# Kernel optimization log

Measured on AMD Instinct MI355X. Metric: run time of the kernel, lower is better.

The kernel has to match this reference:

```python
import jax, jax.numpy as jnp
import numpy as np

D_MODEL = 1024
N_HEADS = 16
D_K = D_MODEL // N_HEADS
B, S = 4, 2048


def setup_inputs() -> dict:
    key = jax.random.key(0)
    ks = jax.random.split(key, 9)
    sc = 1.0 / np.sqrt(D_MODEL)
    inp = {
        "x": jax.random.normal(ks[0], (B, S, D_MODEL), dtype=jnp.float32),
        # causal mask, broadcastable over batch and heads; 0 -> masked
        "mask": jnp.tril(jnp.ones((S, S), dtype=jnp.int32))[None, None, :, :],
        "Wq": jax.random.normal(ks[1], (D_MODEL, D_MODEL), dtype=jnp.float32) * sc,
        "bq": jax.random.normal(ks[2], (D_MODEL,), dtype=jnp.float32) * sc,
        "Wk": jax.random.normal(ks[3], (D_MODEL, D_MODEL), dtype=jnp.float32) * sc,
        "bk": jax.random.normal(ks[4], (D_MODEL,), dtype=jnp.float32) * sc,
        "Wv": jax.random.normal(ks[5], (D_MODEL, D_MODEL), dtype=jnp.float32) * sc,
        "bv": jax.random.normal(ks[6], (D_MODEL,), dtype=jnp.float32) * sc,
        "Wo": jax.random.normal(ks[7], (D_MODEL, D_MODEL), dtype=jnp.float32) * sc,
        "bo": jax.random.normal(ks[8], (D_MODEL,), dtype=jnp.float32) * sc,
    }
    return inp


def _split_heads(t):
    b, s, _ = t.shape
    return t.reshape(b, s, N_HEADS, D_K).transpose(0, 2, 1, 3)  # [B,H,S,dk]


def reference(x, mask, Wq, bq, Wk, bk, Wv, bv, Wo, bo):
    Q = _split_heads(x @ Wq.T + bq)
    K = _split_heads(x @ Wk.T + bk)
    V = _split_heads(x @ Wv.T + bv)
    scores = jnp.einsum("bhqd,bhkd->bhqk", Q, K) / jnp.sqrt(jnp.float32(D_K))
    scores = jnp.where(mask == 0, jnp.float32(-1e9), scores)
    weights = jax.nn.softmax(scores, axis=-1)
    attn = jnp.einsum("bhqk,bhkd->bhqd", weights, V)  # [B,H,S,dk]
    attn = attn.transpose(0, 2, 1, 3).reshape(x.shape[0], x.shape[1], D_MODEL)
    return attn @ Wo.T + bo
```

## Files before the change

### kernel.cpp

```cpp
#include <hip/hip_runtime.h>
#include <hip/hip_bf16.h>
#include <cstdint>

#define DM   1024
#define NH   16
#define DK   64
#define BB   4
#define SS   2048
#define MTOT (BB * SS)
#define PAD  68

typedef short short8 __attribute__((ext_vector_type(8)));
typedef float f32x4  __attribute__((ext_vector_type(4)));
using u16 = unsigned short;

__device__ inline u16 f2b(float f) {
    union { float f; unsigned int u; } v; v.f = f;
    unsigned int u = v.u;
    u += 0x7fffu + ((u >> 16) & 1u);
    return (u16)(u >> 16);
}
__device__ inline u16 f2b_trunc(float f) {
    union { float f; unsigned int u; } v; v.f = f;
    return (u16)(v.u >> 16);
}
__device__ inline float b2f(u16 s) {
    union { unsigned int u; float f; } v; v.u = ((unsigned int)s) << 16;
    return v.f;
}

__device__ inline void load_lds16(const u16* g, u16* l) {
    __builtin_amdgcn_global_load_lds(
        (const __attribute__((address_space(1))) unsigned int*)g,
        (__attribute__((address_space(3))) unsigned int*)l, 16, 0, 0);
}

struct CvtPtrs {
    const void *x, *Wq, *Wk, *Wv, *Wo, *bq, *bk, *bv, *bo;
    u16 *xb, *Wqb, *Wkb, *Wvb, *Wob, *bqb, *bkb, *bvb, *bob;
};

__global__ void convert_all(CvtPtrs p, int* __restrict__ flag)
{
    __shared__ int cnt;
    if (threadIdx.x == 0) cnt = 0;
    __syncthreads();
    int c = 0;
    for (int i = threadIdx.x; i < 512; i += 256) {
        const int e = (((const u16*)p.x)[i] >> 7) & 0xFF;
        if (e >= 100 && e <= 140) c++;
    }
    atomicAdd(&cnt, c);
    __syncthreads();
    const int isbf = (cnt >= 420) ? 1 : 0;
    if (blockIdx.x == 0 && threadIdx.x == 0) *flag = isbf;
    if (isbf) return;

    const size_t E  = (size_t)MTOT * DM;
    const size_t W1 = (size_t)DM * DM;
    const size_t i = ((size_t)blockIdx.x * blockDim.x + threadIdx.x) * 8;
    const float* s; u16* d; size_t off;
    if (i < E) {
        s = (const float*)p.x; d = p.xb; off = i;
    } else {
        size_t j = i - E;
        if (j < (W1 << 2)) {
            const int w = (int)(j >> 20); off = j & (W1 - 1);
            const float* ss[4] = {(const float*)p.Wq, (const float*)p.Wk,
                                  (const float*)p.Wv, (const float*)p.Wo};
            u16* dd[4] = {p.Wqb, p.Wkb, p.Wvb, p.Wob};
            s = ss[w]; d = dd[w];
        } else {
            j -= (W1 << 2);
            if (j >= 4 * DM) return;
            const int w = (int)(j >> 10); off = j & (DM - 1);
            const float* ss[4] = {(const float*)p.bq, (const float*)p.bk,
                                  (const float*)p.bv, (const float*)p.bo};
            u16* dd[4] = {p.bqb, p.bkb, p.bvb, p.bob};
            s = ss[w]; d = dd[w];
        }
    }
    const float4 f0 = *(const float4*)(s + off);
    const float4 f1 = *(const float4*)(s + off + 4);
    u16 tmp[8] = {f2b(f0.x), f2b(f0.y), f2b(f0.z), f2b(f0.w),
                  f2b(f1.x), f2b(f1.y), f2b(f1.z), f2b(f1.w)};
    *(int4*)(d + off) = *(const int4*)tmp;
}

__device__ __forceinline__
void gemm_body(const u16* __restrict__ A, const u16* __restrict__ Bw,
               const u16* __restrict__ bias, void* __restrict__ out,
               int mode, float scale, int isbf, int m0, int n0,
               u16 (*As)[64], u16 (*Bs)[64])
{
    const int tid  = threadIdx.x;
    const int wave = tid >> 6;
    const int lane = tid & 63;
    const int wm = (wave >> 1) * 64;
    const int wn = (wave & 1) * 64;

    const int lm   = lane & 15;
    const int quad = lane >> 4;
    const int kq   = quad * 8;
    const int rq   = quad * 4;

    const int lrow   = lane >> 3;
    const int lchunk = (lane & 7) ^ lrow;
    const u16* gA = A  + (size_t)(m0 + 8*wave + lrow) * DM + lchunk * 8;
    const u16* gB = Bw + (size_t)(n0 + 8*wave + lrow) * DM + lchunk * 8;
    u16* ldsA = (u16*)((char*)&As[0][0] + wave * 1024);
    u16* ldsB = (u16*)((char*)&Bs[0][0] + wave * 1024);

    f32x4 acc[4][4] = {};

    for (int k0 = 0; k0 < DM; k0 += 64) {
        __syncthreads();
#pragma unroll
        for (int c = 0; c < 4; c++) {
            load_lds16(gA + (size_t)c*32*DM + k0, (u16*)((char*)ldsA + c*4096));
            load_lds16(gB + (size_t)c*32*DM + k0, (u16*)((char*)ldsB + c*4096));
        }
        __syncthreads();

#pragma unroll
        for (int ks = 0; ks < 2; ks++) {
            const int ca = ((ks*4 + quad) ^ (lm & 7)) * 8;
            short8 af[4], bf[4];
#pragma unroll
            for (int i = 0; i < 4; i++) af[i] = *(const short8*)(&As[wm + 16*i + lm][ca]);
#pragma unroll
            for (int j = 0; j < 4; j++) bf[j] = *(const short8*)(&Bs[wn + 16*j + lm][ca]);
#pragma unroll
            for (int i = 0; i < 4; i++)
#pragma unroll
                for (int j = 0; j < 4; j++)
                    acc[i][j] = __builtin_amdgcn_mfma_f32_16x16x32_bf16(af[i], bf[j], acc[i][j], 0, 0, 0);
        }
    }

#pragma unroll
    for (int j = 0; j < 4; j++) {
        const int col = n0 + wn + 16*j + lm;
        const float bv = b2f(bias[col]);
        const int h = col >> 6, d = col & 63;
#pragma unroll
        for (int i = 0; i < 4; i++) {
            if (mode == 2) {
                const int row0 = m0 + wm + 16*i + rq;
                const int b = row0 >> 11, s = row0 & 2047;
                u16 tmp[4];
#pragma unroll
                for (int r = 0; r < 4; r++)
                    tmp[r] = f2b((acc[i][j][r] + bv) * scale);
                const size_t idx = (((size_t)(b*NH + h) * DK) + d) * SS + s;
                *(uint2*)(&((u16*)out)[idx]) = *(const uint2*)tmp;
            } else {
#pragma unroll
                for (int r = 0; r < 4; r++) {
                    const int row = m0 + wm + 16*i + rq + r;
                    const float v = (acc[i][j][r] + bv) * scale;
                    if (mode == 0) {
                        const size_t idx = (size_t)row * DM + col;
                        if (isbf) ((u16*)out)[idx] = f2b(v);
                        else      ((float*)out)[idx] = v;
                    } else {
                        const int b = row >> 11, s = row & 2047;
                        const size_t idx = (((size_t)(b*NH + h) * SS) + s) * DK + d;
                        ((u16*)out)[idx] = f2b(v);
                    }
                }
            }
        }
    }
}

__global__ __launch_bounds__(256)
void gemm_qkv(CvtPtrs p, u16* __restrict__ Qb, u16* __restrict__ Kb,
              u16* __restrict__ Vb, float qscale, const int* __restrict__ flag)
{
    __shared__ __align__(16) u16 As[128][64];
    __shared__ __align__(16) u16 Bs[128][64];
    const int id  = blockIdx.x;
    const int xcd = id & 7;
    const int j   = id >> 3;
    const int m0  = (xcd * 8 + (j & 7)) * 128;
    const int n0  = ((j >> 3) & 7) * 128;
    const int z   = j >> 6;
    const int isbf = *flag;
    const u16* A = isbf ? (const u16*)p.x : p.xb;
    const u16* Bw, *bias; u16* out;
    if (z == 0)      { Bw = isbf ? (const u16*)p.Wq : p.Wqb; bias = isbf ? (const u16*)p.bq : p.bqb; out = Qb; }
    else if (z == 1) { Bw = isbf ? (const u16*)p.Wk : p.Wkb; bias = isbf ? (const u16*)p.bk : p.bkb; out = Kb; }
    else             { Bw = isbf ? (const u16*)p.Wv : p.Wvb; bias = isbf ? (const u16*)p.bv : p.bvb; out = Vb; }
    const int mode  = (z == 2) ? 2 : 1;
    const float sc  = (z == 0) ? qscale : 1.0f;
    gemm_body(A, Bw, bias, out, mode, sc, 1, m0, n0, As, Bs);
}

__global__ __launch_bounds__(256)
void gemm_out(const u16* __restrict__ Ab, CvtPtrs p, void* __restrict__ out,
              const int* __restrict__ flag)
{
    __shared__ __align__(16) u16 As[128][64];
    __shared__ __align__(16) u16 Bs[128][64];
    const int id  = blockIdx.x;
    const int xcd = id & 7;
    const int j   = id >> 3;
    const int m0  = (xcd * 8 + (j & 7)) * 128;
    const int n0  = (j >> 3) * 128;
    const int isbf = *flag;
    const u16* Bw   = isbf ? (const u16*)p.Wo : p.Wob;
    const u16* bias = isbf ? (const u16*)p.bo : p.bob;
    gemm_body(Ab, Bw, bias, out, 0, 1.0f, isbf, m0, n0, As, Bs);
}

__global__ __launch_bounds__(256)
void attn_causal(const u16* __restrict__ Q, const u16* __restrict__ K,
                 const u16* __restrict__ VT, u16* __restrict__ O)
{
    __shared__ __align__(16) u16 Ks[2][64][PAD];
    __shared__ __align__(16) u16 Vs[2][64][PAD];
    __shared__ __align__(16) u16 Ps[128][PAD];

    const int tid  = threadIdx.x;
    const int wave = tid >> 6;
    const int lane = tid & 63;
    const int qx = blockIdx.x;
    const int h = blockIdx.y, b = blockIdx.z;
    const int bh = b * NH + h;

    const u16* Kg = K  + (size_t)bh * SS * DK;
    const u16* Vg = VT + (size_t)bh * DK * SS;

    const int srow = tid >> 3;
    const int scol = (tid & 7) * 8;
    const int lm = lane & 15, quad = lane >> 4, kq = quad * 8, rq = quad * 4;

#pragma unroll
    for (int seg = 0; seg < 2; seg++) {
        const int qt = seg ? (15 - qx) : qx;
        const int q0 = qt * 128;
        const int nt = 2 * (qt + 1);
        const u16* Qg = Q + ((size_t)bh * SS + q0) * DK;

        short8 qa[2][2];
#pragma unroll
        for (int mi = 0; mi < 2; mi++)
#pragma unroll
            for (int ks = 0; ks < 2; ks++)
                qa[mi][ks] = *(const short8*)(&Qg[(size_t)(32*wave + 16*mi + lm) * DK + ks*32 + kq]);

        int4 kv0 = *(const int4*)(&Kg[(size_t)srow * DK + scol]);
        int4 kv1 = *(const int4*)(&Kg[(size_t)(srow + 32) * DK + scol]);
        int4 vv0 = *(const int4*)(&Vg[(size_t)srow * SS + scol]);
        int4 vv1 = *(const int4*)(&Vg[(size_t)(srow + 32) * SS + scol]);
        *(int4*)(&Ks[0][srow][scol])      = kv0;
        *(int4*)(&Ks[0][srow + 32][scol]) = kv1;
        *(int4*)(&Vs[0][srow][scol])      = vv0;
        *(int4*)(&Vs[0][srow + 32][scol]) = vv1;
        __syncthreads();

        kv0 = *(const int4*)(&Kg[(size_t)(64 + srow) * DK + scol]);
        kv1 = *(const int4*)(&Kg[(size_t)(64 + srow + 32) * DK + scol]);
        vv0 = *(const int4*)(&Vg[(size_t)srow * SS + 64 + scol]);
        vv1 = *(const int4*)(&Vg[(size_t)(srow + 32) * SS + 64 + scol]);

        f32x4 o[2][4] = {};
        float lacc[2][4] = {};

        for (int t = 0; t < nt; t++) {
            const int buf = t & 1;
            const int k0 = 64 * t;

            f32x4 sc[2][4] = {};
#pragma unroll
            for (int ks = 0; ks < 2; ks++)
#pragma unroll
                for (int j = 0; j < 4; j++) {
                    const short8 bfr = *(const short8*)(&Ks[buf][16*j + lm][ks*32 + kq]);
                    sc[0][j] = __builtin_amdgcn_mfma_f32_16x16x32_bf16(qa[0][ks], bfr, sc[0][j], 0, 0, 0);
                    sc[1][j] = __builtin_amdgcn_mfma_f32_16x16x32_bf16(qa[1][ks], bfr, sc[1][j], 0, 0, 0);
                }

            if (k0 + 63 > q0 + 32*wave) {
#pragma unroll
                for (int mi = 0; mi < 2; mi++)
#pragma unroll
                    for (int j = 0; j < 4; j++)
#pragma unroll
                        for (int r = 0; r < 4; r++)
                            if (k0 + 16*j + lm > q0 + 32*wave + 16*mi + rq + r)
                                sc[mi][j][r] = -1e30f;
            }

#pragma unroll
            for (int mi = 0; mi < 2; mi++)
#pragma unroll
                for (int j = 0; j < 4; j++)
#pragma unroll
                    for (int r = 0; r < 4; r++) {
                        const float pv = __builtin_amdgcn_exp2f(sc[mi][j][r]);
                        lacc[mi][r] += pv;
                        Ps[32*wave + 16*mi + rq + r][16*j + lm] = f2b_trunc(pv);
                    }

#pragma unroll
            for (int ks = 0; ks < 2; ks++) {
                const short8 pa0 = *(const short8*)(&Ps[32*wave + lm][ks*32 + kq]);
                const short8 pa1 = *(const short8*)(&Ps[32*wave + 16 + lm][ks*32 + kq]);
#pragma unroll
                for (int j = 0; j < 4; j++) {
                    const short8 vfr = *(const short8*)(&Vs[buf][16*j + lm][ks*32 + kq]);
                    o[0][j] = __builtin_amdgcn_mfma_f32_16x16x32_bf16(pa0, vfr, o[0][j], 0, 0, 0);
                    o[1][j] = __builtin_amdgcn_mfma_f32_16x16x32_bf16(pa1, vfr, o[1][j], 0, 0, 0);
                }
            }

            if (t + 1 < nt) {
                const int nb = buf ^ 1;
                *(int4*)(&Ks[nb][srow][scol])      = kv0;
                *(int4*)(&Ks[nb][srow + 32][scol]) = kv1;
                *(int4*)(&Vs[nb][srow][scol])      = vv0;
                *(int4*)(&Vs[nb][srow + 32][scol]) = vv1;
                if (t + 2 < nt) {
                    const int kn = 64 * (t + 2);
                    kv0 = *(const int4*)(&Kg[(size_t)(kn + srow) * DK + scol]);
                    kv1 = *(const int4*)(&Kg[(size_t)(kn + srow + 32) * DK + scol]);
                    vv0 = *(const int4*)(&Vg[(size_t)srow * SS + kn + scol]);
                    vv1 = *(const int4*)(&Vg[(size_t)(srow + 32) * SS + kn + scol]);
                }
            }
            __syncthreads();
        }

#pragma unroll
        for (int mi = 0; mi < 2; mi++)
#pragma unroll
            for (int r = 0; r < 4; r++) {
                float v = lacc[mi][r];
#pragma unroll
                for (int off = 1; off < 16; off <<= 1)
                    v += __shfl_xor(v, off, 64);
                const float inv = 1.f / v;
                const size_t rowg = (size_t)b * SS + q0 + 32*wave + 16*mi + rq + r;
#pragma unroll
                for (int j = 0; j < 4; j++)
                    O[rowg * DM + h*DK + 16*j + lm] = f2b(o[mi][j][r] * inv);
            }
    }
}

extern "C" void kernel_launch(void* const* d_in, const int* in_sizes, int n_in,
                              void* d_out, int out_size, void* d_ws, size_t ws_size,
                              hipStream_t stream)
{
    (void)in_sizes; (void)n_in; (void)out_size; (void)ws_size;

    int* flag = (int*)d_ws;
    u16* ws = (u16*)((char*)d_ws + 16);

    const size_t E  = (size_t)MTOT * DM;
    const size_t W1 = (size_t)DM * DM;
    u16* xb  = ws;
    u16* Wqb = ws + E;
    u16* Wkb = Wqb + W1;
    u16* Wvb = Wkb + W1;
    u16* Wob = Wvb + W1;
    u16* bqb = Wob + W1;
    u16* bkb = bqb + DM;
    u16* bvb = bkb + DM;
    u16* bob = bvb + DM;
    u16* Qb  = bob + DM;
    u16* Kb  = Qb + E;
    u16* Vb  = Kb + E;
    u16* Ab  = xb;

    CvtPtrs p;
    p.x = d_in[0];
    p.Wq = d_in[2]; p.bq = d_in[3];
    p.Wk = d_in[4]; p.bk = d_in[5];
    p.Wv = d_in[6]; p.bv = d_in[7];
    p.Wo = d_in[8]; p.bo = d_in[9];
    p.xb = xb;
    p.Wqb = Wqb; p.Wkb = Wkb; p.Wvb = Wvb; p.Wob = Wob;
    p.bqb = bqb; p.bkb = bkb; p.bvb = bvb; p.bob = bob;

    const int cvt_blocks = (int)((E + 4*W1 + 4*DM) / 2048);
    convert_all<<<cvt_blocks, 256, 0, stream>>>(p, flag);

    const float qscale = 0.18033688011112042f;

    gemm_qkv<<<1536, 256, 0, stream>>>(p, Qb, Kb, Vb, qscale, flag);
    attn_causal<<<dim3(SS/256, NH, BB), 256, 0, stream>>>(Qb, Kb, Vb, Ab);
    gemm_out<<<512, 256, 0, stream>>>(Ab, p, d_out, flag);
}
```

Measured before the change: 291.7 us.

## Rewrite projection GEMMs as 8-wave double-buffered pipelined kernels with larger tiles

Replaces the 4-wave 128x128 GEMM body with an 8-wave kernel using 256x256 tiles for QKV and 128x256 tiles for the output projection. LDS is double-buffered, and the next k-slice is prefetched through global_load_lds in quarter stages interleaved with MFMA phases, using manual vmcnt waits, barriers and s_setprio. The aim is to overlap global loads with compute and to raise operand reuse per block. In exchange it uses much more LDS per block (up to 128KB for QKV), which may limit occupancy, and relies on fragile hand-placed waitcnt and barrier synchronisation.

New measurement: 308.5 us. 5.8% more time.

```diff
diff --git a/kernel.cpp b/kernel.cpp
--- a/kernel.cpp
+++ b/kernel.cpp
@@ -34,6 +34,10 @@
         (const __attribute__((address_space(1))) unsigned int*)g,
         (__attribute__((address_space(3))) unsigned int*)l, 16, 0, 0);
 }
+
+#define BARRIER()  __builtin_amdgcn_s_barrier()
+#define WAITVM4()  asm volatile("s_waitcnt vmcnt(4)" ::: "memory")
+#define WAITVM0()  asm volatile("s_waitcnt vmcnt(0)" ::: "memory")
 
 struct CvtPtrs {
     const void *x, *Wq, *Wk, *Wv, *Wo, *bq, *bk, *bv, *bo;
@@ -87,78 +91,169 @@
     *(int4*)(d + off) = *(const int4*)tmp;
 }
 
+template<int ROWS>
 __device__ __forceinline__
-void gemm_body(const u16* __restrict__ A, const u16* __restrict__ Bw,
-               const u16* __restrict__ bias, void* __restrict__ out,
-               int mode, float scale, int isbf, int m0, int n0,
-               u16 (*As)[64], u16 (*Bs)[64])
-{
+void stage_half(const u16* __restrict__ g, int grow0, int k0,
+                u16 (*lds)[64], int r0, int wave, int lane)
+{
+    const int lrow  = lane >> 3;
+    const int chunk = (lane & 7) ^ lrow;
+#pragma unroll
+    for (int i2 = 0; i2 < ROWS / 64; i2++) {
+        const u16* src = g + (size_t)(grow0 + 64*i2 + 8*wave + lrow) * DM
+                           + k0 + chunk * 8;
+        load_lds16(src, &lds[r0 + 64*i2 + 8*wave][0]);
+    }
+}
+
+__device__ __forceinline__
+short8 lds_frag(u16 (*t)[64], int row, int kc)
+{
+    return *(const short8*)(&t[row][(kc ^ (row & 7)) * 8]);
+}
+
+template<int BM>
+__device__ __forceinline__
+void gemm_body8p(const u16* __restrict__ A, const u16* __restrict__ Bw,
+                 const u16* __restrict__ bias, void* __restrict__ out,
+                 int mode, float scale, int isbf, int m0, int n0,
+                 u16 (*As)[64], u16 (*Bs)[64])
+{
+    constexpr int BMW = BM / 2;
+    constexpr int MQ  = BM / 64;
     const int tid  = threadIdx.x;
     const int wave = tid >> 6;
     const int lane = tid & 63;
-    const int wm = (wave >> 1) * 64;
-    const int wn = (wave & 1) * 64;
-
-    const int lm   = lane & 15;
-    const int quad = lane >> 4;
-    const int kq   = quad * 8;
-    const int rq   = quad * 4;
-
-    const int lrow   = lane >> 3;
-    const int lchunk = (lane & 7) ^ lrow;
-    const u16* gA = A  + (size_t)(m0 + 8*wave + lrow) * DM + lchunk * 8;
-    const u16* gB = Bw + (size_t)(n0 + 8*wave + lrow) * DM + lchunk * 8;
-    u16* ldsA = (u16*)((char*)&As[0][0] + wave * 1024);
-    u16* ldsB = (u16*)((char*)&Bs[0][0] + wave * 1024);
-
-    f32x4 acc[4][4] = {};
-
-    for (int k0 = 0; k0 < DM; k0 += 64) {
-        __syncthreads();
-#pragma unroll
-        for (int c = 0; c < 4; c++) {
-            load_lds16(gA + (size_t)c*32*DM + k0, (u16*)((char*)ldsA + c*4096));
-            load_lds16(gB + (size_t)c*32*DM + k0, (u16*)((char*)ldsB + c*4096));
-        }
-        __syncthreads();
-
-#pragma unroll
-        for (int ks = 0; ks < 2; ks++) {
-            const int ca = ((ks*4 + quad) ^ (lm & 7)) * 8;
-            short8 af[4], bf[4];
-#pragma unroll
-            for (int i = 0; i < 4; i++) af[i] = *(const short8*)(&As[wm + 16*i + lm][ca]);
-#pragma unroll
-            for (int j = 0; j < 4; j++) bf[j] = *(const short8*)(&Bs[wn + 16*j + lm][ca]);
-#pragma unroll
-            for (int i = 0; i < 4; i++)
-#pragma unroll
-                for (int j = 0; j < 4; j++)
-                    acc[i][j] = __builtin_amdgcn_mfma_f32_16x16x32_bf16(af[i], bf[j], acc[i][j], 0, 0, 0);
-        }
+    const int wm = wave >> 2;
+    const int wn = wave & 3;
+    const int lm = lane & 15, quad = lane >> 4, rq = quad * 4;
+    const int ar0 = wm * BMW;
+    const int br0 = wn * 64;
+
+    const u16* Ag = A  + (size_t)m0 * DM;
+    const u16* Bg = Bw + (size_t)n0 * DM;
+    u16 (*As0)[64] = As;  u16 (*As1)[64] = As + BM;
+    u16 (*Bs0)[64] = Bs;  u16 (*Bs1)[64] = Bs + 256;
+
+    stage_half<BMW>(Ag, 0,   0,  As0, 0,   wave, lane);
+    stage_half<BMW>(Ag, BMW, 0,  As0, BMW, wave, lane);
+    stage_half<128>(Bg, 0,   0,  Bs0, 0,   wave, lane);
+    stage_half<128>(Bg, 128, 0,  Bs0, 128, wave, lane);
+    stage_half<128>(Bg, 0,   64, Bs1, 0,   wave, lane);
+    stage_half<128>(Bg, 128, 64, Bs1, 128, wave, lane);
+    WAITVM4();
+    BARRIER();
+
+    f32x4 acc[2*MQ][4] = {};
+
+#pragma unroll 2
+    for (int t = 0; t < 16; ++t) {
+        u16 (*Al)[64] = (t & 1) ? As1 : As0;
+        u16 (*Bl)[64] = (t & 1) ? Bs1 : Bs0;
+        u16 (*An)[64] = (t & 1) ? As0 : As1;
+        const int kn1 = (t + 1) * 64, kn2 = (t + 2) * 64;
+
+        short8 af[MQ][2], bA[2][2], bB[2][2];
+
+#pragma unroll
+        for (int i = 0; i < MQ; i++)
+#pragma unroll
+            for (int ks = 0; ks < 2; ks++)
+                af[i][ks] = lds_frag(Al, ar0 + 16*i + lm, ks*4 + quad);
+#pragma unroll
+        for (int j = 0; j < 2; j++)
+#pragma unroll
+            for (int ks = 0; ks < 2; ks++)
+                bA[j][ks] = lds_frag(Bl, br0 + 16*j + lm, ks*4 + quad);
+        if (t + 1 < 16) stage_half<BMW>(Ag, 0, kn1, An, 0, wave, lane);
+        BARRIER();
+        __builtin_amdgcn_s_setprio(1);
+#pragma unroll
+        for (int i = 0; i < MQ; i++)
+#pragma unroll
+            for (int j = 0; j < 2; j++)
+#pragma unroll
+                for (int ks = 0; ks < 2; ks++)
+                    acc[i][j] = __builtin_amdgcn_mfma_f32_16x16x32_bf16(
+                        af[i][ks], bA[j][ks], acc[i][j], 0, 0, 0);
+        __builtin_amdgcn_s_setprio(0);
+        BARRIER();
+
+#pragma unroll
+        for (int j = 0; j < 2; j++)
+#pragma unroll
+            for (int ks = 0; ks < 2; ks++)
+                bB[j][ks] = lds_frag(Bl, br0 + 32 + 16*j + lm, ks*4 + quad);
+        if (t + 1 < 16) stage_half<BMW>(Ag, BMW, kn1, An, BMW, wave, lane);
+        BARRIER();
+        __builtin_amdgcn_s_setprio(1);
+#pragma unroll
+        for (int i = 0; i < MQ; i++)
+#pragma unroll
+            for (int j = 0; j < 2; j++)
+#pragma unroll
+                for (int ks = 0; ks < 2; ks++)
+                    acc[i][2+j] = __builtin_amdgcn_mfma_f32_16x16x32_bf16(
+                        af[i][ks], bB[j][ks], acc[i][2+j], 0, 0, 0);
+        __builtin_amdgcn_s_setprio(0);
+        BARRIER();
+
+#pragma unroll
+        for (int i = 0; i < MQ; i++)
+#pragma unroll
+            for (int ks = 0; ks < 2; ks++)
+                af[i][ks] = lds_frag(Al, ar0 + MQ*16 + 16*i + lm, ks*4 + quad);
+        if (t + 2 < 16) stage_half<128>(Bg, 0, kn2, Bl, 0, wave, lane);
+        BARRIER();
+        __builtin_amdgcn_s_setprio(1);
+#pragma unroll
+        for (int i = 0; i < MQ; i++)
+#pragma unroll
+            for (int j = 0; j < 2; j++)
+#pragma unroll
+                for (int ks = 0; ks < 2; ks++)
+                    acc[MQ+i][2+j] = __builtin_amdgcn_mfma_f32_16x16x32_bf16(
+                        af[i][ks], bB[j][ks], acc[MQ+i][2+j], 0, 0, 0);
+        __builtin_amdgcn_s_setprio(0);
+        BARRIER();
+
+        if (t + 2 < 16) stage_half<128>(Bg, 128, kn2, Bl, 128, wave, lane);
+        BARRIER();
+        __builtin_amdgcn_s_setprio(1);
+#pragma unroll
+        for (int i = 0; i < MQ; i++)
+#pragma unroll
+            for (int j = 0; j < 2; j++)
+#pragma unroll
+                for (int ks = 0; ks < 2; ks++)
+                    acc[MQ+i][j] = __builtin_amdgcn_mfma_f32_16x16x32_bf16(
+                        af[i][ks], bA[j][ks], acc[MQ+i][j], 0, 0, 0);
+        __builtin_amdgcn_s_setprio(0);
+        if (t < 14) WAITVM4(); else WAITVM0();
+        BARRIER();
     }
 
 #pragma unroll
     for (int j = 0; j < 4; j++) {
-        const int col = n0 + wn + 16*j + lm;
-        const float bv = b2f(bias[col]);
+        const int col = n0 + wn*64 + 16*j + lm;
+        const float bvl = b2f(bias[col]);
         const int h = col >> 6, d = col & 63;
 #pragma unroll
-        for (int i = 0; i < 4; i++) {
+        for (int i = 0; i < 2*MQ; i++) {
             if (mode == 2) {
-                const int row0 = m0 + wm + 16*i + rq;
+                const int row0 = m0 + wm*BMW + 16*i + rq;
                 const int b = row0 >> 11, s = row0 & 2047;
                 u16 tmp[4];
 #pragma unroll
                 for (int r = 0; r < 4; r++)
-                    tmp[r] = f2b((acc[i][j][r] + bv) * scale);
+                    tmp[r] = f2b((acc[i][j][r] + bvl) * scale);
                 const size_t idx = (((size_t)(b*NH + h) * DK) + d) * SS + s;
                 *(uint2*)(&((u16*)out)[idx]) = *(const uint2*)tmp;
             } else {
 #pragma unroll
                 for (int r = 0; r < 4; r++) {
-                    const int row = m0 + wm + 16*i + rq + r;
-                    const float v = (acc[i][j][r] + bv) * scale;
+                    const int row = m0 + wm*BMW + 16*i + rq + r;
+                    const float v = (acc[i][j][r] + bvl) * scale;
                     if (mode == 0) {
                         const size_t idx = (size_t)row * DM + col;
                         if (isbf) ((u16*)out)[idx] = f2b(v);
@@ -174,44 +269,43 @@
     }
 }
 
-__global__ __launch_bounds__(256)
+__global__ __launch_bounds__(512, 2)
 void gemm_qkv(CvtPtrs p, u16* __restrict__ Qb, u16* __restrict__ Kb,
               u16* __restrict__ Vb, float qscale, const int* __restrict__ flag)
 {
-    __shared__ __align__(16) u16 As[128][64];
-    __shared__ __align__(16) u16 Bs[128][64];
+    __shared__ __align__(16) u16 As[512][64];
+    __shared__ __align__(16) u16 Bs[512][64];
     const int id  = blockIdx.x;
     const int xcd = id & 7;
-    const int j   = id >> 3;
-    const int m0  = (xcd * 8 + (j & 7)) * 128;
-    const int n0  = ((j >> 3) & 7) * 128;
-    const int z   = j >> 6;
+    const int jb  = id >> 3;
+    const int m0  = (xcd*4 + (jb & 3)) * 256;
+    const int nti = jb >> 2;
+    const int z   = nti >> 2;
+    const int n0  = (nti & 3) * 256;
     const int isbf = *flag;
     const u16* A = isbf ? (const u16*)p.x : p.xb;
-    const u16* Bw, *bias; u16* out;
-    if (z == 0)      { Bw = isbf ? (const u16*)p.Wq : p.Wqb; bias = isbf ? (const u16*)p.bq : p.bqb; out = Qb; }
-    else if (z == 1) { Bw = isbf ? (const u16*)p.Wk : p.Wkb; bias = isbf ? (const u16*)p.bk : p.bkb; out = Kb; }
-    else             { Bw = isbf ? (const u16*)p.Wv : p.Wvb; bias = isbf ? (const u16*)p.bv : p.bvb; out = Vb; }
-    const int mode  = (z == 2) ? 2 : 1;
-    const float sc  = (z == 0) ? qscale : 1.0f;
-    gemm_body(A, Bw, bias, out, mode, sc, 1, m0, n0, As, Bs);
-}
-
-__global__ __launch_bounds__(256)
+    const u16 *Bw, *bias; u16* out; int mode; float sc;
+    if (z == 0)      { Bw = isbf ? (const u16*)p.Wq : p.Wqb; bias = isbf ? (const u16*)p.bq : p.bqb; out = Qb; mode = 1; sc = qscale; }
+    else if (z == 1) { Bw = isbf ? (const u16*)p.Wk : p.Wkb; bias = isbf ? (const u16*)p.bk : p.bkb; out = Kb; mode = 1; sc = 1.0f; }
+    else             { Bw = isbf ? (const u16*)p.Wv : p.Wvb; bias = isbf ? (const u16*)p.bv : p.bvb; out = Vb; mode = 2; sc = 1.0f; }
+    gemm_body8p<256>(A, Bw, bias, out, mode, sc, 1, m0, n0, As, Bs);
+}
+
+__global__ __launch_bounds__(512, 2)
 void gemm_out(const u16* __restrict__ Ab, CvtPtrs p, void* __restrict__ out,
               const int* __restrict__ flag)
 {
-    __shared__ __align__(16) u16 As[128][64];
-    __shared__ __align__(16) u16 Bs[128][64];
+    __shared__ __align__(16) u16 As[256][64];
+    __shared__ __align__(16) u16 Bs[512][64];
     const int id  = blockIdx.x;
     const int xcd = id & 7;
-    const int j   = id >> 3;
-    const int m0  = (xcd * 8 + (j & 7)) * 128;
-    const int n0  = (j >> 3) * 128;
+    const int jb  = id >> 3;
+    const int m0  = (xcd*8 + (jb & 7)) * 128;
+    const int n0  = (jb >> 3) * 256;
     const int isbf = *flag;
     const u16* Bw   = isbf ? (const u16*)p.Wo : p.Wob;
     const u16* bias = isbf ? (const u16*)p.bo : p.bob;
-    gemm_body(Ab, Bw, bias, out, 0, 1.0f, isbf, m0, n0, As, Bs);
+    gemm_body8p<128>(Ab, Bw, bias, out, 0, 1.0f, isbf, m0, n0, As, Bs);
 }
 
 __global__ __launch_bounds__(256)
@@ -390,7 +484,7 @@
 
     const float qscale = 0.18033688011112042f;
 
-    gemm_qkv<<<1536, 256, 0, stream>>>(p, Qb, Kb, Vb, qscale, flag);
+    gemm_qkv<<<384, 512, 0, stream>>>(p, Qb, Kb, Vb, qscale, flag);
     attn_causal<<<dim3(SS/256, NH, BB), 256, 0, stream>>>(Qb, Kb, Vb, Ab);
-    gemm_out<<<512, 256, 0, stream>>>(Ab, p, d_out, flag);
-}
+    gemm_out<<<256, 512, 0, stream>>>(Ab, p, d_out, flag);
+}
```

## Stage GEMM and attention epilogues through LDS for coalesced vector stores

Applied to the files above, without the earlier changes.

The GEMM epilogue for Q/K head-split and output modes now writes results into swizzled shared memory per wave, then emits 16-byte row-contiguous global stores instead of scattered 2- or 4-byte stores. The fp32 output path does the same in two halves using float4 stores. The attention kernel's output is also staged through its P buffer before vectorized row stores. This aims to reduce uncoalesced global write traffic, at the cost of an extra barrier and LDS round trip.

Result: slower. 311.4 us (+6.7%).

```diff
diff --git a/kernel.cpp b/kernel.cpp
--- a/kernel.cpp
+++ b/kernel.cpp
@@ -138,37 +138,85 @@
         }
     }
 
-#pragma unroll
-    for (int j = 0; j < 4; j++) {
-        const int col = n0 + wn + 16*j + lm;
-        const float bv = b2f(bias[col]);
-        const int h = col >> 6, d = col & 63;
-#pragma unroll
-        for (int i = 0; i < 4; i++) {
-            if (mode == 2) {
+    if (mode == 2) {
+#pragma unroll
+        for (int j = 0; j < 4; j++) {
+            const int col = n0 + wn + 16*j + lm;
+            const float bvl = b2f(bias[col]);
+            const int h = col >> 6, d = col & 63;
+#pragma unroll
+            for (int i = 0; i < 4; i++) {
                 const int row0 = m0 + wm + 16*i + rq;
                 const int b = row0 >> 11, s = row0 & 2047;
                 u16 tmp[4];
 #pragma unroll
                 for (int r = 0; r < 4; r++)
-                    tmp[r] = f2b((acc[i][j][r] + bv) * scale);
+                    tmp[r] = f2b((acc[i][j][r] + bvl) * scale);
                 const size_t idx = (((size_t)(b*NH + h) * DK) + d) * SS + s;
                 *(uint2*)(&((u16*)out)[idx]) = *(const uint2*)tmp;
-            } else {
+            }
+        }
+        return;
+    }
+
+    __syncthreads();
+    u16* flat = &As[0][0];
+
+    if (mode == 1 || isbf) {
+        u16* ep = flat + wave * 4096;
+#pragma unroll
+        for (int j = 0; j < 4; j++) {
+            const int col = n0 + wn + 16*j + lm;
+            const float bvl = b2f(bias[col]);
+            const int cl = 16*j + lm;
+#pragma unroll
+            for (int i = 0; i < 4; i++)
 #pragma unroll
                 for (int r = 0; r < 4; r++) {
-                    const int row = m0 + wm + 16*i + rq + r;
-                    const float v = (acc[i][j][r] + bv) * scale;
-                    if (mode == 0) {
-                        const size_t idx = (size_t)row * DM + col;
-                        if (isbf) ((u16*)out)[idx] = f2b(v);
-                        else      ((float*)out)[idx] = v;
-                    } else {
-                        const int b = row >> 11, s = row & 2047;
-                        const size_t idx = (((size_t)(b*NH + h) * SS) + s) * DK + d;
-                        ((u16*)out)[idx] = f2b(v);
+                    const int rl = 16*i + rq + r;
+                    ep[rl*64 + (((cl >> 3) ^ (rl & 7)) * 8) + (cl & 7)] =
+                        f2b((acc[i][j][r] + bvl) * scale);
+                }
+        }
+        const int rl = lane;
+        const int grow = m0 + wm + rl;
+        u16* ob;
+        if (mode == 1) {
+            const int h = (n0 + wn) >> 6;
+            const int b = grow >> 11, s = grow & 2047;
+            ob = (u16*)out + (((size_t)(b*NH + h) * SS) + s) * DK;
+        } else {
+            ob = (u16*)out + (size_t)grow * DM + (n0 + wn);
+        }
+#pragma unroll
+        for (int c = 0; c < 8; c++)
+            *(short8*)(ob + c*8) = *(const short8*)(ep + rl*64 + ((c ^ (rl & 7)) * 8));
+    } else {
+        float* epf = (float*)flat + wave * 2048;
+#pragma unroll
+        for (int hp = 0; hp < 2; hp++) {
+#pragma unroll
+            for (int j = 0; j < 4; j++) {
+                const int col = n0 + wn + 16*j + lm;
+                const float bvl = b2f(bias[col]);
+                const int cl = 16*j + lm;
+#pragma unroll
+                for (int i2 = 0; i2 < 2; i2++)
+#pragma unroll
+                    for (int r = 0; r < 4; r++) {
+                        const int rl = 16*i2 + rq + r;
+                        epf[rl*64 + (((cl >> 2) ^ (rl & 15)) * 4) + (cl & 3)] =
+                            acc[2*hp + i2][j][r] + bvl;
                     }
-                }
+            }
+            const int rl = lane >> 1, hh = lane & 1;
+            const int grow = m0 + wm + 32*hp + rl;
+            float* ob = (float*)out + (size_t)grow * DM + (n0 + wn);
+#pragma unroll
+            for (int c = 0; c < 8; c++) {
+                const int sc = hh*8 + c;
+                *(float4*)(ob + sc*4) =
+                    *(const float4*)(epf + rl*64 + ((sc ^ (rl & 15)) * 4));
             }
         }
     }
@@ -178,8 +226,7 @@
 void gemm_qkv(CvtPtrs p, u16* __restrict__ Qb, u16* __restrict__ Kb,
               u16* __restrict__ Vb, float qscale, const int* __restrict__ flag)
 {
-    __shared__ __align__(16) u16 As[128][64];
-    __shared__ __align__(16) u16 Bs[128][64];
+    __shared__ __align__(16) u16 SM[2][128][64];
     const int id  = blockIdx.x;
     const int xcd = id & 7;
     const int j   = id >> 3;
@@ -194,15 +241,14 @@
     else             { Bw = isbf ? (const u16*)p.Wv : p.Wvb; bias = isbf ? (const u16*)p.bv : p.bvb; out = Vb; }
     const int mode  = (z == 2) ? 2 : 1;
     const float sc  = (z == 0) ? qscale : 1.0f;
-    gemm_body(A, Bw, bias, out, mode, sc, 1, m0, n0, As, Bs);
+    gemm_body(A, Bw, bias, out, mode, sc, 1, m0, n0, SM[0], SM[1]);
 }
 
 __global__ __launch_bounds__(256)
 void gemm_out(const u16* __restrict__ Ab, CvtPtrs p, void* __restrict__ out,
               const int* __restrict__ flag)
 {
-    __shared__ __align__(16) u16 As[128][64];
-    __shared__ __align__(16) u16 Bs[128][64];
+    __shared__ __align__(16) u16 SM[2][128][64];
     const int id  = blockIdx.x;
     const int xcd = id & 7;
     const int j   = id >> 3;
@@ -211,7 +257,7 @@
     const int isbf = *flag;
     const u16* Bw   = isbf ? (const u16*)p.Wo : p.Wob;
     const u16* bias = isbf ? (const u16*)p.bo : p.bob;
-    gemm_body(Ab, Bw, bias, out, 0, 1.0f, isbf, m0, n0, As, Bs);
+    gemm_body(Ab, Bw, bias, out, 0, 1.0f, isbf, m0, n0, SM[0], SM[1]);
 }
 
 __global__ __launch_bounds__(256)
@@ -342,11 +388,18 @@
                 for (int off = 1; off < 16; off <<= 1)
                     v += __shfl_xor(v, off, 64);
                 const float inv = 1.f / v;
-                const size_t rowg = (size_t)b * SS + q0 + 32*wave + 16*mi + rq + r;
 #pragma unroll
                 for (int j = 0; j < 4; j++)
-                    O[rowg * DM + h*DK + 16*j + lm] = f2b(o[mi][j][r] * inv);
-            }
+                    Ps[32*wave + 16*mi + rq + r][16*j + lm] = f2b(o[mi][j][r] * inv);
+            }
+        {
+            const int rl = lane >> 1, hh = lane & 1;
+            const size_t rowg = (size_t)b * SS + q0 + 32*wave + rl;
+            u16* ob = O + rowg * DM + h*DK + hh*32;
+#pragma unroll
+            for (int c = 0; c < 4; c++)
+                *(short8*)(ob + c*8) = *(const short8*)(&Ps[32*wave + rl][hh*32 + c*8]);
+        }
     }
 }
 
```
